# Kernel tuning notes

Hardware: AMD Instinct MI355X
Metric: run time of the kernel (lower is better)

## Reference

```python
import jax, jax.numpy as jnp
import numpy as np

N_NODES = 100000
N_EDGES = 3200000
N_FEAT = 512
NHID = 256
LATENT = 64

def _spmm(edge_index, edge_weight, h, num_nodes):
    # out[dst] = sum_e w_e * h[src_e]  (sparse adj @ h)
    src, dst = edge_index[0], edge_index[1]
    msgs = edge_weight[:, None] * h[src]            # [E, D]
    return jax.ops.segment_sum(msgs, dst, num_segments=num_nodes)

def _gcn_conv(x, edge_index, edge_weight, W, b, num_nodes):
    # GCNConv: adj @ (x @ W) + b
    return _spmm(edge_index, edge_weight, x @ W, num_nodes) + b

def setup_inputs() -> dict:
    key = jax.random.key(0)
    ks = jax.random.split(key, 8)
    x = jax.random.normal(ks[0], (N_NODES, N_FEAT), dtype=jnp.float32)
    edge_index = jax.random.randint(ks[1], (2, N_EDGES), 0, N_NODES, dtype=jnp.int32)
    edge_weight = jax.random.uniform(ks[2], (N_EDGES,), dtype=jnp.float32)
    s1 = 1.0 / np.sqrt(N_FEAT)
    s2 = 1.0 / np.sqrt(NHID)
    W1 = jax.random.normal(ks[3], (N_FEAT, NHID), dtype=jnp.float32) * s1
    b1 = jnp.zeros((NHID,), dtype=jnp.float32)
    W_mu = jax.random.normal(ks[4], (NHID, LATENT), dtype=jnp.float32) * s2
    b_mu = jnp.zeros((LATENT,), dtype=jnp.float32)
    W_logvar = jax.random.normal(ks[5], (NHID, LATENT), dtype=jnp.float32) * s2
    b_logvar = jnp.zeros((LATENT,), dtype=jnp.float32)
    return {"x": x, "edge_index": edge_index, "edge_weight": edge_weight,
            "W1": W1, "b1": b1, "W_mu": W_mu, "b_mu": b_mu,
            "W_logvar": W_logvar, "b_logvar": b_logvar}

def reference(x, edge_index, edge_weight, W1, b1, W_mu, b_mu, W_logvar, b_logvar):
    n = x.shape[0]
    # dropout is identity in eval mode (training=False)
    h = jax.nn.relu(_gcn_conv(x, edge_index, edge_weight, W1, b1, n))  # [N, nhid]
    mu = _gcn_conv(h, edge_index, edge_weight, W_mu, b_mu, n)          # [N, latent]
    logvar = _gcn_conv(h, edge_index, edge_weight, W_logvar, b_logvar, n)
    return (mu, logvar)
```

## Files before the change

### kernel.cpp

```cpp
#include <hip/hip_runtime.h>
#include <hip/hip_bf16.h>

#define NN 100000
#define NE 3200000
#define NF 512
#define NH 256
#define NL 64
#define PAD 40

#define NBKT 256
#define NPB 391
#define CAP 13500
#define NCLS 16
#define DIVC 6250

typedef __bf16 bf16x8 __attribute__((ext_vector_type(8)));
typedef __bf16 bf16x4 __attribute__((ext_vector_type(4)));
typedef __bf16 bf16x2 __attribute__((ext_vector_type(2)));
typedef float  f32x4  __attribute__((ext_vector_type(4)));

__global__ void k_binit2(int* __restrict__ bcur) {
    int t = threadIdx.x;
    bcur[t * 16] = t * CAP;
}

__global__ __launch_bounds__(256) void k_bucket0(const int* __restrict__ src,
                                                 const int* __restrict__ dst,
                                                 const int* __restrict__ wbits,
                                                 int* __restrict__ bcur,
                                                 int2* __restrict__ stage_sw,
                                                 int* __restrict__ stage_d) {
    __shared__ int cnt[NBKT];
    __shared__ int base[NBKT];
    int tid = threadIdx.x;
    cnt[tid] = 0;
    __syncthreads();
    int e0 = blockIdx.x * 1024;
    int ss[4], ww[4], dd[4], lr[4], bb[4];
#pragma unroll
    for (int k = 0; k < 4; k++) {
        int e = e0 + k * 256 + tid;
        int d = dst[e];
        int s = src[e];
        ss[k] = s;
        ww[k] = wbits[e];
        int cls = (int)((unsigned)s / DIVC);
        dd[k] = d | (cls << 20);
        bb[k] = (int)((unsigned)d / NPB);
        lr[k] = atomicAdd(&cnt[bb[k]], 1);
    }
    __syncthreads();
    base[tid] = atomicAdd(&bcur[tid * 16], cnt[tid]);
    __syncthreads();
#pragma unroll
    for (int k = 0; k < 4; k++) {
        int pos = base[bb[k]] + lr[k];
        stage_sw[pos] = make_int2(ss[k], ww[k]);
        stage_d[pos] = dd[k];
    }
}

__global__ void k_bscan(const int* __restrict__ bcur, int* __restrict__ bstart) {
    __shared__ int s[NBKT];
    int t = threadIdx.x;
    int v = bcur[t * 16] - t * CAP;
    s[t] = v;
    __syncthreads();
    for (int off = 1; off < NBKT; off <<= 1) {
        int a = (t >= off) ? s[t - off] : 0;
        __syncthreads();
        s[t] += a;
        __syncthreads();
    }
    bstart[t] = s[t] - v;
    if (t == NBKT - 1) bstart[NBKT] = s[t];
}

__global__ __launch_bounds__(512) void k_build(const int2* __restrict__ stage_sw,
                                               const int* __restrict__ stage_d,
                                               const int* __restrict__ bcur,
                                               const int* __restrict__ bstart,
                                               int* __restrict__ deg,
                                               int* __restrict__ row_ptr,
                                               int2* __restrict__ sedge) {
    __shared__ int hist2[NPB * NCLS];
    __shared__ int sb[2][512];
    int b = blockIdx.x;
    int t = threadIdx.x;
    int n0 = b * NPB;
    int nb = NN - n0; if (nb > NPB) nb = NPB;
    int s0 = b * CAP;
    int fill = bcur[b * 16] - s0;

    for (int i = t; i < nb * NCLS; i += 512) hist2[i] = 0;
    __syncthreads();
    for (int i = t; i < fill; i += 512) {
        int v = stage_d[s0 + i];
        atomicAdd(&hist2[(v & 0xFFFFF) - n0 + ((v >> 20) * 0)], 1);
    }
    __syncthreads();
    for (int i = t; i < nb * NCLS; i += 512) hist2[i] = 0;
    __syncthreads();
    for (int i = t; i < fill; i += 512) {
        int v = stage_d[s0 + i];
        int dn = (v & 0xFFFFF) - n0;
        int c = v >> 20;
        atomicAdd(&hist2[dn * NCLS + c], 1);
    }
    __syncthreads();
    int tot = 0;
    if (t < nb) {
#pragma unroll
        for (int c = 0; c < NCLS; c++) tot += hist2[t * NCLS + c];
    }
    sb[0][t] = (t < nb) ? tot : 0;
    __syncthreads();
    int cur = 0;
    for (int off = 1; off < 512; off <<= 1) {
        int nv = sb[cur][t] + ((t >= off) ? sb[cur][t - off] : 0);
        cur ^= 1;
        sb[cur][t] = nv;
        __syncthreads();
    }
    int base = bstart[b];
    if (t < nb) {
        int acc = base + sb[cur][t] - tot;
        deg[n0 + t] = tot;
        row_ptr[n0 + t] = acc;
#pragma unroll
        for (int c = 0; c < NCLS; c++) {
            int tmp = hist2[t * NCLS + c];
            hist2[t * NCLS + c] = acc;
            acc += tmp;
        }
    }
    __syncthreads();
    for (int i = t; i < fill; i += 512) {
        int v = stage_d[s0 + i];
        int dn = (v & 0xFFFFF) - n0;
        int c = v >> 20;
        int pos = atomicAdd(&hist2[dn * NCLS + c], 1);
        sedge[pos] = stage_sw[s0 + i];
    }
}

__global__ void k_packW1(const float* __restrict__ W, __bf16* __restrict__ P) {
    int i = blockIdx.x * 256 + threadIdx.x;
    int j = i & 7, l = (i >> 3) & 63, kc = (i >> 9) & 15, nt = i >> 13;
    int k = kc * 32 + (l >> 4) * 8 + j;
    int n = nt * 16 + (l & 15);
    P[i] = (__bf16)W[k * NH + n];
}

__global__ void k_packW2(const float* __restrict__ Wmu, const float* __restrict__ Wlv,
                         __bf16* __restrict__ P) {
    int i = blockIdx.x * 256 + threadIdx.x;
    int j = i & 7, l = (i >> 3) & 63, kc = (i >> 9) & 7, nt = i >> 12;
    int k = kc * 32 + (l >> 4) * 8 + j;
    int n = nt * 16 + (l & 15);
    float v = (n < NL) ? Wmu[k * NL + n] : Wlv[k * NL + (n - NL)];
    P[i] = (__bf16)v;
}

__global__ __launch_bounds__(256) void k_gemm1(const float* __restrict__ x,
                                               const __bf16* __restrict__ Wp,
                                               __bf16* __restrict__ T) {
    __shared__ __bf16 As[64 * PAD];
    int tid = threadIdx.x;
    int wv = tid >> 6, lane = tid & 63;
    int quad = lane >> 4, l16 = lane & 15;
    long m0 = (long)blockIdx.x * 64;

    int srow = tid >> 2;
    int scol = (tid & 3) * 8;
    long grow = m0 + srow; if (grow > NN - 1) grow = NN - 1;
    const float* xrow = x + grow * NF;

    f32x4 acc[4][4];
#pragma unroll
    for (int a = 0; a < 4; a++)
#pragma unroll
        for (int b = 0; b < 4; b++) acc[a][b] = (f32x4)0.f;

    float4 p0 = *(const float4*)(xrow + scol);
    float4 p1 = *(const float4*)(xrow + scol + 4);

    for (int kc = 0; kc < 16; kc++) {
        union { bf16x8 v; __bf16 e[8]; } u;
        u.e[0] = (__bf16)p0.x; u.e[1] = (__bf16)p0.y;
        u.e[2] = (__bf16)p0.z; u.e[3] = (__bf16)p0.w;
        u.e[4] = (__bf16)p1.x; u.e[5] = (__bf16)p1.y;
        u.e[6] = (__bf16)p1.z; u.e[7] = (__bf16)p1.w;
        *(bf16x8*)&As[srow * PAD + scol] = u.v;
        __syncthreads();
        if (kc < 15) {
            p0 = *(const float4*)(xrow + (kc + 1) * 32 + scol);
            p1 = *(const float4*)(xrow + (kc + 1) * 32 + scol + 4);
        }
        bf16x8 bfr[4];
#pragma unroll
        for (int nt = 0; nt < 4; nt++)
            bfr[nt] = *(const bf16x8*)(Wp + (((long)(wv * 4 + nt) * 16 + kc) * 64 + lane) * 8);
#pragma unroll
        for (int mt = 0; mt < 4; mt++) {
            bf16x8 af = *(const bf16x8*)&As[(mt * 16 + l16) * PAD + quad * 8];
#pragma unroll
            for (int nt = 0; nt < 4; nt++)
                acc[mt][nt] = __builtin_amdgcn_mfma_f32_16x16x32_bf16(af, bfr[nt], acc[mt][nt], 0, 0, 0);
        }
        __syncthreads();
    }
#pragma unroll
    for (int mt = 0; mt < 4; mt++)
#pragma unroll
        for (int r = 0; r < 4; r++) {
            long gr = m0 + mt * 16 + quad * 4 + r;
            if (gr < NN) {
#pragma unroll
                for (int nt = 0; nt < 4; nt++)
                    T[gr * 256 + wv * 64 + nt * 16 + l16] = (__bf16)acc[mt][nt][r];
            }
        }
}

__global__ __launch_bounds__(256) void k_spmm_h(const __bf16* __restrict__ T,
                                                const int2* __restrict__ sedge,
                                                const int* __restrict__ row_ptr,
                                                const int* __restrict__ deg,
                                                const float* __restrict__ bias,
                                                __bf16* __restrict__ o) {
    int wave = threadIdx.x >> 6, lane = threadIdx.x & 63;
    int n = blockIdx.x * 4 + wave;
    if (n >= NN) return;
    int i = row_ptr[n];
    int end = i + deg[n];
    float a0 = 0.f, a1 = 0.f, a2 = 0.f, a3 = 0.f;
    const bf16x4* base = (const bf16x4*)T;
    for (; i + 8 <= end; i += 8) {
        int2 e0 = sedge[i], e1 = sedge[i+1], e2 = sedge[i+2], e3 = sedge[i+3];
        int2 e4 = sedge[i+4], e5 = sedge[i+5], e6 = sedge[i+6], e7 = sedge[i+7];
        bf16x4 v0 = base[(long)e0.x * 64 + lane];
        bf16x4 v1 = base[(long)e1.x * 64 + lane];
        bf16x4 v2 = base[(long)e2.x * 64 + lane];
        bf16x4 v3 = base[(long)e3.x * 64 + lane];
        bf16x4 v4 = base[(long)e4.x * 64 + lane];
        bf16x4 v5 = base[(long)e5.x * 64 + lane];
        bf16x4 v6 = base[(long)e6.x * 64 + lane];
        bf16x4 v7 = base[(long)e7.x * 64 + lane];
        float w0 = __uint_as_float(e0.y), w1 = __uint_as_float(e1.y);
        float w2 = __uint_as_float(e2.y), w3 = __uint_as_float(e3.y);
        float w4 = __uint_as_float(e4.y), w5 = __uint_as_float(e5.y);
        float w6 = __uint_as_float(e6.y), w7 = __uint_as_float(e7.y);
        a0 += w0*(float)v0[0] + w1*(float)v1[0] + w2*(float)v2[0] + w3*(float)v3[0]
            + w4*(float)v4[0] + w5*(float)v5[0] + w6*(float)v6[0] + w7*(float)v7[0];
        a1 += w0*(float)v0[1] + w1*(float)v1[1] + w2*(float)v2[1] + w3*(float)v3[1]
            + w4*(float)v4[1] + w5*(float)v5[1] + w6*(float)v6[1] + w7*(float)v7[1];
        a2 += w0*(float)v0[2] + w1*(float)v1[2] + w2*(float)v2[2] + w3*(float)v3[2]
            + w4*(float)v4[2] + w5*(float)v5[2] + w6*(float)v6[2] + w7*(float)v7[2];
        a3 += w0*(float)v0[3] + w1*(float)v1[3] + w2*(float)v2[3] + w3*(float)v3[3]
            + w4*(float)v4[3] + w5*(float)v5[3] + w6*(float)v6[3] + w7*(float)v7[3];
    }
    for (; i < end; i++) {
        int2 e = sedge[i];
        float w = __uint_as_float(e.y);
        bf16x4 v = base[(long)e.x * 64 + lane];
        a0 += w*(float)v[0]; a1 += w*(float)v[1];
        a2 += w*(float)v[2]; a3 += w*(float)v[3];
    }
    float4 bv = ((const float4*)bias)[lane];
    bf16x4 ov;
    ov[0] = (__bf16)fmaxf(a0 + bv.x, 0.f);
    ov[1] = (__bf16)fmaxf(a1 + bv.y, 0.f);
    ov[2] = (__bf16)fmaxf(a2 + bv.z, 0.f);
    ov[3] = (__bf16)fmaxf(a3 + bv.w, 0.f);
    ((bf16x4*)o)[(long)n * 64 + lane] = ov;
}

__global__ __launch_bounds__(256) void k_gemm2(const __bf16* __restrict__ h,
                                               const __bf16* __restrict__ Wp,
                                               __bf16* __restrict__ HMb) {
    __shared__ __bf16 As[128 * PAD];
    int tid = threadIdx.x;
    int wv = tid >> 6, lane = tid & 63;
    int quad = lane >> 4, l16 = lane & 15;
    int wr = (wv >> 1) * 64, wc = (wv & 1) * 64;
    long m0 = (long)blockIdx.x * 128;

    int srow = tid >> 1;
    int scol = (tid & 1) * 16;
    long grow = m0 + srow; if (grow > NN - 1) grow = NN - 1;

    f32x4 acc[4][4];
#pragma unroll
    for (int a = 0; a < 4; a++)
#pragma unroll
        for (int b = 0; b < 4; b++) acc[a][b] = (f32x4)0.f;

    const __bf16* rH = h + grow * 256;
    bf16x8 p0 = *(const bf16x8*)(rH + scol);
    bf16x8 p1 = *(const bf16x8*)(rH + scol + 8);

    for (int kc = 0; kc < 8; kc++) {
        *(bf16x8*)&As[srow * PAD + scol] = p0;
        *(bf16x8*)&As[srow * PAD + scol + 8] = p1;
        __syncthreads();
        if (kc < 7) {
            const __bf16* nxt = rH + (kc + 1) * 32;
            p0 = *(const bf16x8*)(nxt + scol);
            p1 = *(const bf16x8*)(nxt + scol + 8);
        }
        bf16x8 bfr[4];
#pragma unroll
        for (int nt = 0; nt < 4; nt++) {
            int ntg = (wc >> 4) + nt;
            bfr[nt] = *(const bf16x8*)(Wp + (((long)ntg * 8 + kc) * 64 + lane) * 8);
        }
#pragma unroll
        for (int mt = 0; mt < 4; mt++) {
            bf16x8 af = *(const bf16x8*)&As[(wr + mt * 16 + l16) * PAD + quad * 8];
#pragma unroll
            for (int nt = 0; nt < 4; nt++)
                acc[mt][nt] = __builtin_amdgcn_mfma_f32_16x16x32_bf16(af, bfr[nt], acc[mt][nt], 0, 0, 0);
        }
        __syncthreads();
    }
#pragma unroll
    for (int mt = 0; mt < 4; mt++)
#pragma unroll
        for (int r = 0; r < 4; r++) {
            long gr = m0 + wr + mt * 16 + quad * 4 + r;
            if (gr < NN) {
#pragma unroll
                for (int nt = 0; nt < 4; nt++)
                    HMb[gr * 128 + wc + nt * 16 + l16] = (__bf16)acc[mt][nt][r];
            }
        }
}

__global__ __launch_bounds__(256) void k_spmm2(const __bf16* __restrict__ HMb,
                                               const int2* __restrict__ sedge,
                                               const int* __restrict__ row_ptr,
                                               const int* __restrict__ deg,
                                               const float* __restrict__ bmu,
                                               const float* __restrict__ blv,
                                               float* __restrict__ out) {
    int wave = threadIdx.x >> 6, lane = threadIdx.x & 63;
    int n = blockIdx.x * 4 + wave;
    if (n >= NN) return;
    int i = row_ptr[n];
    int end = i + deg[n];
    float a0 = 0.f, a1 = 0.f;
    const bf16x2* base = (const bf16x2*)HMb;
    for (; i + 8 <= end; i += 8) {
        int2 e0 = sedge[i], e1 = sedge[i+1], e2 = sedge[i+2], e3 = sedge[i+3];
        int2 e4 = sedge[i+4], e5 = sedge[i+5], e6 = sedge[i+6], e7 = sedge[i+7];
        bf16x2 v0 = base[(long)e0.x * 64 + lane];
        bf16x2 v1 = base[(long)e1.x * 64 + lane];
        bf16x2 v2 = base[(long)e2.x * 64 + lane];
        bf16x2 v3 = base[(long)e3.x * 64 + lane];
        bf16x2 v4 = base[(long)e4.x * 64 + lane];
        bf16x2 v5 = base[(long)e5.x * 64 + lane];
        bf16x2 v6 = base[(long)e6.x * 64 + lane];
        bf16x2 v7 = base[(long)e7.x * 64 + lane];
        a0 += __uint_as_float(e0.y) * (float)v0[0] + __uint_as_float(e1.y) * (float)v1[0]
            + __uint_as_float(e2.y) * (float)v2[0] + __uint_as_float(e3.y) * (float)v3[0]
            + __uint_as_float(e4.y) * (float)v4[0] + __uint_as_float(e5.y) * (float)v5[0]
            + __uint_as_float(e6.y) * (float)v6[0] + __uint_as_float(e7.y) * (float)v7[0];
        a1 += __uint_as_float(e0.y) * (float)v0[1] + __uint_as_float(e1.y) * (float)v1[1]
            + __uint_as_float(e2.y) * (float)v2[1] + __uint_as_float(e3.y) * (float)v3[1]
            + __uint_as_float(e4.y) * (float)v4[1] + __uint_as_float(e5.y) * (float)v5[1]
            + __uint_as_float(e6.y) * (float)v6[1] + __uint_as_float(e7.y) * (float)v7[1];
    }
    for (; i < end; i++) {
        int2 e = sedge[i];
        float w = __uint_as_float(e.y);
        bf16x2 v = base[(long)e.x * 64 + lane];
        a0 += w * (float)v[0]; a1 += w * (float)v[1];
    }
    if (lane < 32) {
        float2 b = ((const float2*)bmu)[lane];
        float2 o = {a0 + b.x, a1 + b.y};
        ((float2*)out)[(long)n * 32 + lane] = o;
    } else {
        float2 b = ((const float2*)blv)[lane - 32];
        float2 o = {a0 + b.x, a1 + b.y};
        ((float2*)(out + (long)NN * NL))[(long)n * 32 + (lane - 32)] = o;
    }
}

extern "C" void kernel_launch(void* const* d_in, const int* in_sizes, int n_in,
                              void* d_out, int out_size, void* d_ws, size_t ws_size,
                              hipStream_t stream) {
    const float* x   = (const float*)d_in[0];
    const int*   ei  = (const int*)d_in[1];
    const float* ew  = (const float*)d_in[2];
    const float* W1  = (const float*)d_in[3];
    const float* b1  = (const float*)d_in[4];
    const float* Wmu = (const float*)d_in[5];
    const float* bmu = (const float*)d_in[6];
    const float* Wlv = (const float*)d_in[7];
    const float* blv = (const float*)d_in[8];
    float* out = (float*)d_out;

    char* ws = (char*)d_ws;
    __bf16* XW     = (__bf16*)(ws);
    __bf16* h      = (__bf16*)(ws + 51200000);
    __bf16* HMb    = (__bf16*)(ws + 102400000);
    int2*  sedge   = (int2*) (ws + 128000000);
    int*   deg     = (int*)  (ws + 153600000);
    int*   row_ptr = (int*)  (ws + 154000000);
    int*   bcur    = (int*)  (ws + 154400000);
    int*   bstart  = (int*)  (ws + 154800000);
    __bf16* Wp1    = (__bf16*)(ws + 154900000);
    __bf16* Wp2    = (__bf16*)(ws + 155200000);

    int2* stage_sw = (int2*)(ws + 51200000);
    int*  stage_d  = (int*) (ws + 51200000 + (long)NBKT * CAP * 8);

    const int* esrc = ei;
    const int* edst = ei + NE;

    k_packW1<<<dim3(512), dim3(256), 0, stream>>>(W1, Wp1);
    k_packW2<<<dim3(128), dim3(256), 0, stream>>>(Wmu, Wlv, Wp2);

    k_binit2<<<dim3(1), dim3(NBKT), 0, stream>>>(bcur);
    k_bucket0<<<dim3(NE / 1024), dim3(256), 0, stream>>>(esrc, edst, (const int*)ew,
                                                         bcur, stage_sw, stage_d);
    k_bscan<<<dim3(1), dim3(NBKT), 0, stream>>>(bcur, bstart);
    k_build<<<dim3(NBKT), dim3(512), 0, stream>>>(stage_sw, stage_d, bcur, bstart,
                                                  deg, row_ptr, sedge);

    k_gemm1<<<dim3((NN + 63) / 64), dim3(256), 0, stream>>>(x, Wp1, XW);
    k_spmm_h<<<dim3((NN + 3) / 4), dim3(256), 0, stream>>>(XW, sedge, row_ptr, deg, b1, h);

    k_gemm2<<<dim3((NN + 127) / 128), dim3(256), 0, stream>>>(h, Wp2, HMb);
    k_spmm2<<<dim3((NN + 3) / 4), dim3(256), 0, stream>>>(HMb, sedge, row_ptr, deg, bmu, blv, out);
}
```

Measured before the change: 842.7 us.

## Process 8-row groups per wave with LDS accumulators, sorting edges by source class

Edges are bucketed into groups of eight destination rows, and within each group sorted by source class, so one wave walks all edges of a group in source-class order. Gathers from the feature tables therefore sweep source nodes more coherently across the group, which should improve cache locality. Per-row partial sums live in LDS and are updated with read-modify-write per edge; the local row index is packed into the high bits of the source field. The cost is an LDS read-modify-write per edge plus serialized dependencies when consecutive edges hit the same row. The bucket count and per-bucket node count change to divide evenly into groups.

Measured after the change: 812.3 us. 1.04x faster.

```diff
diff --git a/kernel.cpp b/kernel.cpp
--- a/kernel.cpp
+++ b/kernel.cpp
@@ -8,20 +8,24 @@
 #define NL 64
 #define PAD 40
 
-#define NBKT 256
-#define NPB 391
-#define CAP 13500
+#define NBKT 250
+#define NPB 400
+#define CAP 13600
 #define NCLS 16
 #define DIVC 6250
+#define RPW 8
+#define SGB 50
+#define NSG 12500
 
 typedef __bf16 bf16x8 __attribute__((ext_vector_type(8)));
 typedef __bf16 bf16x4 __attribute__((ext_vector_type(4)));
 typedef __bf16 bf16x2 __attribute__((ext_vector_type(2)));
 typedef float  f32x4  __attribute__((ext_vector_type(4)));
+typedef float  f32x2  __attribute__((ext_vector_type(2)));
 
 __global__ void k_binit2(int* __restrict__ bcur) {
     int t = threadIdx.x;
-    bcur[t * 16] = t * CAP;
+    if (t < NBKT) bcur[t * 16] = t * CAP;
 }
 
 __global__ __launch_bounds__(256) void k_bucket0(const int* __restrict__ src,
@@ -33,7 +37,7 @@
     __shared__ int cnt[NBKT];
     __shared__ int base[NBKT];
     int tid = threadIdx.x;
-    cnt[tid] = 0;
+    if (tid < NBKT) cnt[tid] = 0;
     __syncthreads();
     int e0 = blockIdx.x * 1024;
     int ss[4], ww[4], dd[4], lr[4], bb[4];
@@ -50,7 +54,7 @@
         lr[k] = atomicAdd(&cnt[bb[k]], 1);
     }
     __syncthreads();
-    base[tid] = atomicAdd(&bcur[tid * 16], cnt[tid]);
+    if (tid < NBKT) base[tid] = atomicAdd(&bcur[tid * 16], cnt[tid]);
     __syncthreads();
 #pragma unroll
     for (int k = 0; k < 4; k++) {
@@ -60,87 +64,75 @@
     }
 }
 
-__global__ void k_bscan(const int* __restrict__ bcur, int* __restrict__ bstart) {
-    __shared__ int s[NBKT];
+__global__ void k_bscan(const int* __restrict__ bcur, int* __restrict__ bstart,
+                        int* __restrict__ run_off) {
+    __shared__ int s[256];
     int t = threadIdx.x;
-    int v = bcur[t * 16] - t * CAP;
+    int v = (t < NBKT) ? (bcur[t * 16] - t * CAP) : 0;
     s[t] = v;
     __syncthreads();
-    for (int off = 1; off < NBKT; off <<= 1) {
+    for (int off = 1; off < 256; off <<= 1) {
         int a = (t >= off) ? s[t - off] : 0;
         __syncthreads();
         s[t] += a;
         __syncthreads();
     }
-    bstart[t] = s[t] - v;
-    if (t == NBKT - 1) bstart[NBKT] = s[t];
+    if (t < NBKT) bstart[t] = s[t] - v;
+    if (t == 0) run_off[NSG * NCLS] = NE;
 }
 
 __global__ __launch_bounds__(512) void k_build(const int2* __restrict__ stage_sw,
                                                const int* __restrict__ stage_d,
                                                const int* __restrict__ bcur,
                                                const int* __restrict__ bstart,
-                                               int* __restrict__ deg,
-                                               int* __restrict__ row_ptr,
+                                               int* __restrict__ run_off,
                                                int2* __restrict__ sedge) {
-    __shared__ int hist2[NPB * NCLS];
-    __shared__ int sb[2][512];
+    __shared__ int hist[SGB * NCLS];
+    __shared__ int sgtot[SGB];
+    __shared__ int sgoff[SGB];
     int b = blockIdx.x;
     int t = threadIdx.x;
     int n0 = b * NPB;
-    int nb = NN - n0; if (nb > NPB) nb = NPB;
     int s0 = b * CAP;
     int fill = bcur[b * 16] - s0;
 
-    for (int i = t; i < nb * NCLS; i += 512) hist2[i] = 0;
+    for (int i = t; i < SGB * NCLS; i += 512) hist[i] = 0;
     __syncthreads();
     for (int i = t; i < fill; i += 512) {
         int v = stage_d[s0 + i];
-        atomicAdd(&hist2[(v & 0xFFFFF) - n0 + ((v >> 20) * 0)], 1);
-    }
-    __syncthreads();
-    for (int i = t; i < nb * NCLS; i += 512) hist2[i] = 0;
+        int d = v & 0xFFFFF, c = v >> 20;
+        atomicAdd(&hist[((d - n0) >> 3) * NCLS + c], 1);
+    }
+    __syncthreads();
+    if (t < SGB) {
+        int sum = 0;
+#pragma unroll
+        for (int c = 0; c < NCLS; c++) sum += hist[t * NCLS + c];
+        sgtot[t] = sum;
+    }
+    __syncthreads();
+    if (t == 0) {
+        int a = 0;
+        for (int sgi = 0; sgi < SGB; sgi++) { sgoff[sgi] = a; a += sgtot[sgi]; }
+    }
+    __syncthreads();
+    if (t < SGB) {
+        int a = bstart[b] + sgoff[t];
+#pragma unroll
+        for (int c = 0; c < NCLS; c++) {
+            int tmp = hist[t * NCLS + c];
+            hist[t * NCLS + c] = a;
+            run_off[(long)(b * SGB + t) * NCLS + c] = a;
+            a += tmp;
+        }
+    }
     __syncthreads();
     for (int i = t; i < fill; i += 512) {
         int v = stage_d[s0 + i];
-        int dn = (v & 0xFFFFF) - n0;
-        int c = v >> 20;
-        atomicAdd(&hist2[dn * NCLS + c], 1);
-    }
-    __syncthreads();
-    int tot = 0;
-    if (t < nb) {
-#pragma unroll
-        for (int c = 0; c < NCLS; c++) tot += hist2[t * NCLS + c];
-    }
-    sb[0][t] = (t < nb) ? tot : 0;
-    __syncthreads();
-    int cur = 0;
-    for (int off = 1; off < 512; off <<= 1) {
-        int nv = sb[cur][t] + ((t >= off) ? sb[cur][t - off] : 0);
-        cur ^= 1;
-        sb[cur][t] = nv;
-        __syncthreads();
-    }
-    int base = bstart[b];
-    if (t < nb) {
-        int acc = base + sb[cur][t] - tot;
-        deg[n0 + t] = tot;
-        row_ptr[n0 + t] = acc;
-#pragma unroll
-        for (int c = 0; c < NCLS; c++) {
-            int tmp = hist2[t * NCLS + c];
-            hist2[t * NCLS + c] = acc;
-            acc += tmp;
-        }
-    }
-    __syncthreads();
-    for (int i = t; i < fill; i += 512) {
-        int v = stage_d[s0 + i];
-        int dn = (v & 0xFFFFF) - n0;
-        int c = v >> 20;
-        int pos = atomicAdd(&hist2[dn * NCLS + c], 1);
-        sedge[pos] = stage_sw[s0 + i];
+        int d = v & 0xFFFFF, c = v >> 20;
+        int pos = atomicAdd(&hist[((d - n0) >> 3) * NCLS + c], 1);
+        int2 sw = stage_sw[s0 + i];
+        sedge[pos] = make_int2(sw.x | ((d & 7) << 20), sw.y);
     }
 }
 
@@ -223,57 +215,66 @@
         }
 }
 
+#define RMW4(EV, VV) { float w = __uint_as_float(EV.y); \
+    f32x4* a = &A[((EV).x >> 20) * 64 + lane]; f32x4 tt = *a; \
+    tt[0] += w * (float)VV[0]; tt[1] += w * (float)VV[1]; \
+    tt[2] += w * (float)VV[2]; tt[3] += w * (float)VV[3]; *a = tt; }
+
 __global__ __launch_bounds__(256) void k_spmm_h(const __bf16* __restrict__ T,
                                                 const int2* __restrict__ sedge,
-                                                const int* __restrict__ row_ptr,
-                                                const int* __restrict__ deg,
+                                                const int* __restrict__ roff,
                                                 const float* __restrict__ bias,
                                                 __bf16* __restrict__ o) {
-    int wave = threadIdx.x >> 6, lane = threadIdx.x & 63;
-    int n = blockIdx.x * 4 + wave;
-    if (n >= NN) return;
-    int i = row_ptr[n];
-    int end = i + deg[n];
-    float a0 = 0.f, a1 = 0.f, a2 = 0.f, a3 = 0.f;
+    __shared__ f32x4 acc[4][RPW][64];
+    int wv = __builtin_amdgcn_readfirstlane(threadIdx.x >> 6);
+    int lane = threadIdx.x & 63;
+    int sg = blockIdx.x * 4 + wv;
+    f32x4* A = &acc[wv][0][0];
+    for (int i = lane; i < RPW * 64; i += 64) A[i] = (f32x4)0.f;
     const bf16x4* base = (const bf16x4*)T;
-    for (; i + 8 <= end; i += 8) {
-        int2 e0 = sedge[i], e1 = sedge[i+1], e2 = sedge[i+2], e3 = sedge[i+3];
-        int2 e4 = sedge[i+4], e5 = sedge[i+5], e6 = sedge[i+6], e7 = sedge[i+7];
-        bf16x4 v0 = base[(long)e0.x * 64 + lane];
-        bf16x4 v1 = base[(long)e1.x * 64 + lane];
-        bf16x4 v2 = base[(long)e2.x * 64 + lane];
-        bf16x4 v3 = base[(long)e3.x * 64 + lane];
-        bf16x4 v4 = base[(long)e4.x * 64 + lane];
-        bf16x4 v5 = base[(long)e5.x * 64 + lane];
-        bf16x4 v6 = base[(long)e6.x * 64 + lane];
-        bf16x4 v7 = base[(long)e7.x * 64 + lane];
-        float w0 = __uint_as_float(e0.y), w1 = __uint_as_float(e1.y);
-        float w2 = __uint_as_float(e2.y), w3 = __uint_as_float(e3.y);
-        float w4 = __uint_as_float(e4.y), w5 = __uint_as_float(e5.y);
-        float w6 = __uint_as_float(e6.y), w7 = __uint_as_float(e7.y);
-        a0 += w0*(float)v0[0] + w1*(float)v1[0] + w2*(float)v2[0] + w3*(float)v3[0]
-            + w4*(float)v4[0] + w5*(float)v5[0] + w6*(float)v6[0] + w7*(float)v7[0];
-        a1 += w0*(float)v0[1] + w1*(float)v1[1] + w2*(float)v2[1] + w3*(float)v3[1]
-            + w4*(float)v4[1] + w5*(float)v5[1] + w6*(float)v6[1] + w7*(float)v7[1];
-        a2 += w0*(float)v0[2] + w1*(float)v1[2] + w2*(float)v2[2] + w3*(float)v3[2]
-            + w4*(float)v4[2] + w5*(float)v5[2] + w6*(float)v6[2] + w7*(float)v7[2];
-        a3 += w0*(float)v0[3] + w1*(float)v1[3] + w2*(float)v2[3] + w3*(float)v3[3]
-            + w4*(float)v4[3] + w5*(float)v5[3] + w6*(float)v6[3] + w7*(float)v7[3];
-    }
-    for (; i < end; i++) {
-        int2 e = sedge[i];
-        float w = __uint_as_float(e.y);
-        bf16x4 v = base[(long)e.x * 64 + lane];
-        a0 += w*(float)v[0]; a1 += w*(float)v[1];
-        a2 += w*(float)v[2]; a3 += w*(float)v[3];
+    for (int c = 0; c < NCLS; c++) {
+        int i = roff[sg * NCLS + c];
+        int e = roff[sg * NCLS + c + 1];
+        for (; i + 8 <= e; i += 8) {
+            int2 e0 = sedge[i], e1 = sedge[i+1], e2 = sedge[i+2], e3 = sedge[i+3];
+            int2 e4 = sedge[i+4], e5 = sedge[i+5], e6 = sedge[i+6], e7 = sedge[i+7];
+            bf16x4 v0 = base[(long)(e0.x & 0xFFFFF) * 64 + lane];
+            bf16x4 v1 = base[(long)(e1.x & 0xFFFFF) * 64 + lane];
+            bf16x4 v2 = base[(long)(e2.x & 0xFFFFF) * 64 + lane];
+            bf16x4 v3 = base[(long)(e3.x & 0xFFFFF) * 64 + lane];
+            bf16x4 v4 = base[(long)(e4.x & 0xFFFFF) * 64 + lane];
+            bf16x4 v5 = base[(long)(e5.x & 0xFFFFF) * 64 + lane];
+            bf16x4 v6 = base[(long)(e6.x & 0xFFFFF) * 64 + lane];
+            bf16x4 v7 = base[(long)(e7.x & 0xFFFFF) * 64 + lane];
+            RMW4(e0, v0) RMW4(e1, v1) RMW4(e2, v2) RMW4(e3, v3)
+            RMW4(e4, v4) RMW4(e5, v5) RMW4(e6, v6) RMW4(e7, v7)
+        }
+        for (; i + 4 <= e; i += 4) {
+            int2 e0 = sedge[i], e1 = sedge[i+1], e2 = sedge[i+2], e3 = sedge[i+3];
+            bf16x4 v0 = base[(long)(e0.x & 0xFFFFF) * 64 + lane];
+            bf16x4 v1 = base[(long)(e1.x & 0xFFFFF) * 64 + lane];
+            bf16x4 v2 = base[(long)(e2.x & 0xFFFFF) * 64 + lane];
+            bf16x4 v3 = base[(long)(e3.x & 0xFFFFF) * 64 + lane];
+            RMW4(e0, v0) RMW4(e1, v1) RMW4(e2, v2) RMW4(e3, v3)
+        }
+        for (; i < e; i++) {
+            int2 e0 = sedge[i];
+            bf16x4 v0 = base[(long)(e0.x & 0xFFFFF) * 64 + lane];
+            RMW4(e0, v0)
+        }
     }
     float4 bv = ((const float4*)bias)[lane];
-    bf16x4 ov;
-    ov[0] = (__bf16)fmaxf(a0 + bv.x, 0.f);
-    ov[1] = (__bf16)fmaxf(a1 + bv.y, 0.f);
-    ov[2] = (__bf16)fmaxf(a2 + bv.z, 0.f);
-    ov[3] = (__bf16)fmaxf(a3 + bv.w, 0.f);
-    ((bf16x4*)o)[(long)n * 64 + lane] = ov;
+    long n0 = (long)sg * RPW;
+#pragma unroll
+    for (int r = 0; r < RPW; r++) {
+        f32x4 t = A[r * 64 + lane];
+        bf16x4 ov;
+        ov[0] = (__bf16)fmaxf(t[0] + bv.x, 0.f);
+        ov[1] = (__bf16)fmaxf(t[1] + bv.y, 0.f);
+        ov[2] = (__bf16)fmaxf(t[2] + bv.z, 0.f);
+        ov[3] = (__bf16)fmaxf(t[3] + bv.w, 0.f);
+        ((bf16x4*)o)[(n0 + r) * 64 + lane] = ov;
+    }
 }
 
 __global__ __launch_bounds__(256) void k_gemm2(const __bf16* __restrict__ h,
@@ -337,54 +338,68 @@
         }
 }
 
+#define RMW2(EV, VV) { float w = __uint_as_float(EV.y); \
+    f32x2* a = &A[((EV).x >> 20) * 64 + lane]; f32x2 tt = *a; \
+    tt[0] += w * (float)VV[0]; tt[1] += w * (float)VV[1]; *a = tt; }
+
 __global__ __launch_bounds__(256) void k_spmm2(const __bf16* __restrict__ HMb,
                                                const int2* __restrict__ sedge,
-                                               const int* __restrict__ row_ptr,
-                                               const int* __restrict__ deg,
+                                               const int* __restrict__ roff,
                                                const float* __restrict__ bmu,
                                                const float* __restrict__ blv,
                                                float* __restrict__ out) {
-    int wave = threadIdx.x >> 6, lane = threadIdx.x & 63;
-    int n = blockIdx.x * 4 + wave;
-    if (n >= NN) return;
-    int i = row_ptr[n];
-    int end = i + deg[n];
-    float a0 = 0.f, a1 = 0.f;
+    __shared__ f32x2 acc[4][RPW][64];
+    int wv = __builtin_amdgcn_readfirstlane(threadIdx.x >> 6);
+    int lane = threadIdx.x & 63;
+    int sg = blockIdx.x * 4 + wv;
+    f32x2* A = &acc[wv][0][0];
+    for (int i = lane; i < RPW * 64; i += 64) A[i] = (f32x2)0.f;
     const bf16x2* base = (const bf16x2*)HMb;
-    for (; i + 8 <= end; i += 8) {
-        int2 e0 = sedge[i], e1 = sedge[i+1], e2 = sedge[i+2], e3 = sedge[i+3];
-        int2 e4 = sedge[i+4], e5 = sedge[i+5], e6 = sedge[i+6], e7 = sedge[i+7];
-        bf16x2 v0 = base[(long)e0.x * 64 + lane];
-        bf16x2 v1 = base[(long)e1.x * 64 + lane];
-        bf16x2 v2 = base[(long)e2.x * 64 + lane];
-        bf16x2 v3 = base[(long)e3.x * 64 + lane];
-        bf16x2 v4 = base[(long)e4.x * 64 + lane];
-        bf16x2 v5 = base[(long)e5.x * 64 + lane];
-        bf16x2 v6 = base[(long)e6.x * 64 + lane];
-        bf16x2 v7 = base[(long)e7.x * 64 + lane];
-        a0 += __uint_as_float(e0.y) * (float)v0[0] + __uint_as_float(e1.y) * (float)v1[0]
-            + __uint_as_float(e2.y) * (float)v2[0] + __uint_as_float(e3.y) * (float)v3[0]
-            + __uint_as_float(e4.y) * (float)v4[0] + __uint_as_float(e5.y) * (float)v5[0]
-            + __uint_as_float(e6.y) * (float)v6[0] + __uint_as_float(e7.y) * (float)v7[0];
-        a1 += __uint_as_float(e0.y) * (float)v0[1] + __uint_as_float(e1.y) * (float)v1[1]
-            + __uint_as_float(e2.y) * (float)v2[1] + __uint_as_float(e3.y) * (float)v3[1]
-            + __uint_as_float(e4.y) * (float)v4[1] + __uint_as_float(e5.y) * (float)v5[1]
-            + __uint_as_float(e6.y) * (float)v6[1] + __uint_as_float(e7.y) * (float)v7[1];
-    }
-    for (; i < end; i++) {
-        int2 e = sedge[i];
-        float w = __uint_as_float(e.y);
-        bf16x2 v = base[(long)e.x * 64 + lane];
-        a0 += w * (float)v[0]; a1 += w * (float)v[1];
-    }
-    if (lane < 32) {
-        float2 b = ((const float2*)bmu)[lane];
-        float2 o = {a0 + b.x, a1 + b.y};
-        ((float2*)out)[(long)n * 32 + lane] = o;
-    } else {
-        float2 b = ((const float2*)blv)[lane - 32];
-        float2 o = {a0 + b.x, a1 + b.y};
-        ((float2*)(out + (long)NN * NL))[(long)n * 32 + (lane - 32)] = o;
+    for (int c = 0; c < NCLS; c++) {
+        int i = roff[sg * NCLS + c];
+        int e = roff[sg * NCLS + c + 1];
+        for (; i + 8 <= e; i += 8) {
+            int2 e0 = sedge[i], e1 = sedge[i+1], e2 = sedge[i+2], e3 = sedge[i+3];
+            int2 e4 = sedge[i+4], e5 = sedge[i+5], e6 = sedge[i+6], e7 = sedge[i+7];
+            bf16x2 v0 = base[(long)(e0.x & 0xFFFFF) * 64 + lane];
+            bf16x2 v1 = base[(long)(e1.x & 0xFFFFF) * 64 + lane];
+            bf16x2 v2 = base[(long)(e2.x & 0xFFFFF) * 64 + lane];
+            bf16x2 v3 = base[(long)(e3.x & 0xFFFFF) * 64 + lane];
+            bf16x2 v4 = base[(long)(e4.x & 0xFFFFF) * 64 + lane];
+            bf16x2 v5 = base[(long)(e5.x & 0xFFFFF) * 64 + lane];
+            bf16x2 v6 = base[(long)(e6.x & 0xFFFFF) * 64 + lane];
+            bf16x2 v7 = base[(long)(e7.x & 0xFFFFF) * 64 + lane];
+            RMW2(e0, v0) RMW2(e1, v1) RMW2(e2, v2) RMW2(e3, v3)
+            RMW2(e4, v4) RMW2(e5, v5) RMW2(e6, v6) RMW2(e7, v7)
+        }
+        for (; i + 4 <= e; i += 4) {
+            int2 e0 = sedge[i], e1 = sedge[i+1], e2 = sedge[i+2], e3 = sedge[i+3];
+            bf16x2 v0 = base[(long)(e0.x & 0xFFFFF) * 64 + lane];
+            bf16x2 v1 = base[(long)(e1.x & 0xFFFFF) * 64 + lane];
+            bf16x2 v2 = base[(long)(e2.x & 0xFFFFF) * 64 + lane];
+            bf16x2 v3 = base[(long)(e3.x & 0xFFFFF) * 64 + lane];
+            RMW2(e0, v0) RMW2(e1, v1) RMW2(e2, v2) RMW2(e3, v3)
+        }
+        for (; i < e; i++) {
+            int2 e0 = sedge[i];
+            bf16x2 v0 = base[(long)(e0.x & 0xFFFFF) * 64 + lane];
+            RMW2(e0, v0)
+        }
+    }
+    long n0 = (long)sg * RPW;
+#pragma unroll
+    for (int r = 0; r < RPW; r++) {
+        f32x2 t = A[r * 64 + lane];
+        float2 o2;
+        if (lane < 32) {
+            float2 b = ((const float2*)bmu)[lane];
+            o2.x = t[0] + b.x; o2.y = t[1] + b.y;
+            ((float2*)out)[(n0 + r) * 32 + lane] = o2;
+        } else {
+            float2 b = ((const float2*)blv)[lane - 32];
+            o2.x = t[0] + b.x; o2.y = t[1] + b.y;
+            ((float2*)(out + (long)NN * NL))[(n0 + r) * 32 + (lane - 32)] = o2;
+        }
     }
 }
 
@@ -407,15 +422,14 @@
     __bf16* h      = (__bf16*)(ws + 51200000);
     __bf16* HMb    = (__bf16*)(ws + 102400000);
     int2*  sedge   = (int2*) (ws + 128000000);
-    int*   deg     = (int*)  (ws + 153600000);
-    int*   row_ptr = (int*)  (ws + 154000000);
-    int*   bcur    = (int*)  (ws + 154400000);
+    int*   run_off = (int*)  (ws + 153600000);
+    int*   bcur    = (int*)  (ws + 154450000);
     int*   bstart  = (int*)  (ws + 154800000);
     __bf16* Wp1    = (__bf16*)(ws + 154900000);
     __bf16* Wp2    = (__bf16*)(ws + 155200000);
 
     int2* stage_sw = (int2*)(ws + 51200000);
-    int*  stage_d  = (int*) (ws + 51200000 + (long)NBKT * CAP * 8);
+    int*  stage_d  = (int*) (ws + 78400000);
 
     const int* esrc = ei;
     const int* edst = ei + NE;
@@ -423,16 +437,16 @@
     k_packW1<<<dim3(512), dim3(256), 0, stream>>>(W1, Wp1);
     k_packW2<<<dim3(128), dim3(256), 0, stream>>>(Wmu, Wlv, Wp2);
 
-    k_binit2<<<dim3(1), dim3(NBKT), 0, stream>>>(bcur);
+    k_binit2<<<dim3(1), dim3(256), 0, stream>>>(bcur);
     k_bucket0<<<dim3(NE / 1024), dim3(256), 0, stream>>>(esrc, edst, (const int*)ew,
                                                          bcur, stage_sw, stage_d);
-    k_bscan<<<dim3(1), dim3(NBKT), 0, stream>>>(bcur, bstart);
+    k_bscan<<<dim3(1), dim3(256), 0, stream>>>(bcur, bstart, run_off);
     k_build<<<dim3(NBKT), dim3(512), 0, stream>>>(stage_sw, stage_d, bcur, bstart,
-                                                  deg, row_ptr, sedge);
+                                                  run_off, sedge);
 
     k_gemm1<<<dim3((NN + 63) / 64), dim3(256), 0, stream>>>(x, Wp1, XW);
-    k_spmm_h<<<dim3((NN + 3) / 4), dim3(256), 0, stream>>>(XW, sedge, row_ptr, deg, b1, h);
+    k_spmm_h<<<dim3(NSG / 4), dim3(256), 0, stream>>>(XW, sedge, run_off, b1, h);
 
     k_gemm2<<<dim3((NN + 127) / 128), dim3(256), 0, stream>>>(h, Wp2, HMb);
-    k_spmm2<<<dim3((NN + 3) / 4), dim3(256), 0, stream>>>(HMb, sedge, row_ptr, deg, bmu, blv, out);
-}
+    k_spmm2<<<dim3(NSG / 4), dim3(256), 0, stream>>>(HMb, sedge, run_off, bmu, blv, out);
+}
```

## Drop source-class sub-sorting in CSR build and restructure SpMM gather unrolling

Applied to the files above, without the earlier changes.

The CSR build no longer sub-sorts each destination row's edges by source class. It also drops the duplicated histogram pass and uses a single per-node histogram with 250 buckets of 400 nodes. Both SpMM kernels switch from 8-way summed-expression unrolling to 16-way array-based gathers with a 4-way tail loop, so more gather loads can be in flight. The trade-off is that losing the source-class ordering may reduce cache locality of the feature gathers, and the larger unroll raises register pressure.

Measured after the change: 821.4 us. 2.5% less time.

```diff
diff --git a/kernel.cpp b/kernel.cpp
--- a/kernel.cpp
+++ b/kernel.cpp
@@ -8,11 +8,9 @@
 #define NL 64
 #define PAD 40
 
-#define NBKT 256
-#define NPB 391
-#define CAP 13500
-#define NCLS 16
-#define DIVC 6250
+#define NBKT 250
+#define NPB 400
+#define CAP 13600
 
 typedef __bf16 bf16x8 __attribute__((ext_vector_type(8)));
 typedef __bf16 bf16x4 __attribute__((ext_vector_type(4)));
@@ -21,7 +19,7 @@
 
 __global__ void k_binit2(int* __restrict__ bcur) {
     int t = threadIdx.x;
-    bcur[t * 16] = t * CAP;
+    if (t < NBKT) bcur[t * 16] = t * CAP;
 }
 
 __global__ __launch_bounds__(256) void k_bucket0(const int* __restrict__ src,
@@ -33,7 +31,7 @@
     __shared__ int cnt[NBKT];
     __shared__ int base[NBKT];
     int tid = threadIdx.x;
-    cnt[tid] = 0;
+    if (tid < NBKT) cnt[tid] = 0;
     __syncthreads();
     int e0 = blockIdx.x * 1024;
     int ss[4], ww[4], dd[4], lr[4], bb[4];
@@ -41,16 +39,14 @@
     for (int k = 0; k < 4; k++) {
         int e = e0 + k * 256 + tid;
         int d = dst[e];
-        int s = src[e];
-        ss[k] = s;
+        ss[k] = src[e];
         ww[k] = wbits[e];
-        int cls = (int)((unsigned)s / DIVC);
-        dd[k] = d | (cls << 20);
+        dd[k] = d;
         bb[k] = (int)((unsigned)d / NPB);
         lr[k] = atomicAdd(&cnt[bb[k]], 1);
     }
     __syncthreads();
-    base[tid] = atomicAdd(&bcur[tid * 16], cnt[tid]);
+    if (tid < NBKT) base[tid] = atomicAdd(&bcur[tid * 16], cnt[tid]);
     __syncthreads();
 #pragma unroll
     for (int k = 0; k < 4; k++) {
@@ -61,19 +57,18 @@
 }
 
 __global__ void k_bscan(const int* __restrict__ bcur, int* __restrict__ bstart) {
-    __shared__ int s[NBKT];
+    __shared__ int s[256];
     int t = threadIdx.x;
-    int v = bcur[t * 16] - t * CAP;
+    int v = (t < NBKT) ? (bcur[t * 16] - t * CAP) : 0;
     s[t] = v;
     __syncthreads();
-    for (int off = 1; off < NBKT; off <<= 1) {
+    for (int off = 1; off < 256; off <<= 1) {
         int a = (t >= off) ? s[t - off] : 0;
         __syncthreads();
         s[t] += a;
         __syncthreads();
     }
-    bstart[t] = s[t] - v;
-    if (t == NBKT - 1) bstart[NBKT] = s[t];
+    if (t < NBKT) bstart[t] = s[t] - v;
 }
 
 __global__ __launch_bounds__(512) void k_build(const int2* __restrict__ stage_sw,
@@ -83,63 +78,40 @@
                                                int* __restrict__ deg,
                                                int* __restrict__ row_ptr,
                                                int2* __restrict__ sedge) {
-    __shared__ int hist2[NPB * NCLS];
+    __shared__ int hist[NPB];
     __shared__ int sb[2][512];
     int b = blockIdx.x;
     int t = threadIdx.x;
     int n0 = b * NPB;
-    int nb = NN - n0; if (nb > NPB) nb = NPB;
     int s0 = b * CAP;
     int fill = bcur[b * 16] - s0;
 
-    for (int i = t; i < nb * NCLS; i += 512) hist2[i] = 0;
+    if (t < NPB) hist[t] = 0;
+    __syncthreads();
+    for (int i = t; i < fill; i += 512)
+        atomicAdd(&hist[stage_d[s0 + i] - n0], 1);
+    __syncthreads();
+    int v = (t < NPB) ? hist[t] : 0;
+    int buf = 0;
+    sb[0][t] = v;
+    __syncthreads();
+    for (int off = 1; off < 512; off <<= 1) {
+        int nv = sb[buf][t] + ((t >= off) ? sb[buf][t - off] : 0);
+        buf ^= 1;
+        sb[buf][t] = nv;
+        __syncthreads();
+    }
+    int base = bstart[b];
+    if (t < NPB) {
+        int abs0 = base + sb[buf][t] - v;
+        deg[n0 + t] = v;
+        row_ptr[n0 + t] = abs0;
+        hist[t] = abs0;
+    }
     __syncthreads();
     for (int i = t; i < fill; i += 512) {
-        int v = stage_d[s0 + i];
-        atomicAdd(&hist2[(v & 0xFFFFF) - n0 + ((v >> 20) * 0)], 1);
-    }
-    __syncthreads();
-    for (int i = t; i < nb * NCLS; i += 512) hist2[i] = 0;
-    __syncthreads();
-    for (int i = t; i < fill; i += 512) {
-        int v = stage_d[s0 + i];
-        int dn = (v & 0xFFFFF) - n0;
-        int c = v >> 20;
-        atomicAdd(&hist2[dn * NCLS + c], 1);
-    }
-    __syncthreads();
-    int tot = 0;
-    if (t < nb) {
-#pragma unroll
-        for (int c = 0; c < NCLS; c++) tot += hist2[t * NCLS + c];
-    }
-    sb[0][t] = (t < nb) ? tot : 0;
-    __syncthreads();
-    int cur = 0;
-    for (int off = 1; off < 512; off <<= 1) {
-        int nv = sb[cur][t] + ((t >= off) ? sb[cur][t - off] : 0);
-        cur ^= 1;
-        sb[cur][t] = nv;
-        __syncthreads();
-    }
-    int base = bstart[b];
-    if (t < nb) {
-        int acc = base + sb[cur][t] - tot;
-        deg[n0 + t] = tot;
-        row_ptr[n0 + t] = acc;
-#pragma unroll
-        for (int c = 0; c < NCLS; c++) {
-            int tmp = hist2[t * NCLS + c];
-            hist2[t * NCLS + c] = acc;
-            acc += tmp;
-        }
-    }
-    __syncthreads();
-    for (int i = t; i < fill; i += 512) {
-        int v = stage_d[s0 + i];
-        int dn = (v & 0xFFFFF) - n0;
-        int c = v >> 20;
-        int pos = atomicAdd(&hist2[dn * NCLS + c], 1);
+        int dl = stage_d[s0 + i] - n0;
+        int pos = atomicAdd(&hist[dl], 1);
         sedge[pos] = stage_sw[s0 + i];
     }
 }
@@ -236,36 +208,44 @@
     int end = i + deg[n];
     float a0 = 0.f, a1 = 0.f, a2 = 0.f, a3 = 0.f;
     const bf16x4* base = (const bf16x4*)T;
-    for (; i + 8 <= end; i += 8) {
-        int2 e0 = sedge[i], e1 = sedge[i+1], e2 = sedge[i+2], e3 = sedge[i+3];
-        int2 e4 = sedge[i+4], e5 = sedge[i+5], e6 = sedge[i+6], e7 = sedge[i+7];
-        bf16x4 v0 = base[(long)e0.x * 64 + lane];
-        bf16x4 v1 = base[(long)e1.x * 64 + lane];
-        bf16x4 v2 = base[(long)e2.x * 64 + lane];
-        bf16x4 v3 = base[(long)e3.x * 64 + lane];
-        bf16x4 v4 = base[(long)e4.x * 64 + lane];
-        bf16x4 v5 = base[(long)e5.x * 64 + lane];
-        bf16x4 v6 = base[(long)e6.x * 64 + lane];
-        bf16x4 v7 = base[(long)e7.x * 64 + lane];
-        float w0 = __uint_as_float(e0.y), w1 = __uint_as_float(e1.y);
-        float w2 = __uint_as_float(e2.y), w3 = __uint_as_float(e3.y);
-        float w4 = __uint_as_float(e4.y), w5 = __uint_as_float(e5.y);
-        float w6 = __uint_as_float(e6.y), w7 = __uint_as_float(e7.y);
-        a0 += w0*(float)v0[0] + w1*(float)v1[0] + w2*(float)v2[0] + w3*(float)v3[0]
-            + w4*(float)v4[0] + w5*(float)v5[0] + w6*(float)v6[0] + w7*(float)v7[0];
-        a1 += w0*(float)v0[1] + w1*(float)v1[1] + w2*(float)v2[1] + w3*(float)v3[1]
-            + w4*(float)v4[1] + w5*(float)v5[1] + w6*(float)v6[1] + w7*(float)v7[1];
-        a2 += w0*(float)v0[2] + w1*(float)v1[2] + w2*(float)v2[2] + w3*(float)v3[2]
-            + w4*(float)v4[2] + w5*(float)v5[2] + w6*(float)v6[2] + w7*(float)v7[2];
-        a3 += w0*(float)v0[3] + w1*(float)v1[3] + w2*(float)v2[3] + w3*(float)v3[3]
-            + w4*(float)v4[3] + w5*(float)v5[3] + w6*(float)v6[3] + w7*(float)v7[3];
+    for (; i + 16 <= end; i += 16) {
+        int2 e[16];
+#pragma unroll
+        for (int k = 0; k < 16; k++) e[k] = sedge[i + k];
+        bf16x4 v[16];
+#pragma unroll
+        for (int k = 0; k < 16; k++) v[k] = base[(long)e[k].x * 64 + lane];
+#pragma unroll
+        for (int k = 0; k < 16; k++) {
+            float w = __uint_as_float(e[k].y);
+            a0 += w * (float)v[k][0];
+            a1 += w * (float)v[k][1];
+            a2 += w * (float)v[k][2];
+            a3 += w * (float)v[k][3];
+        }
+    }
+    for (; i + 4 <= end; i += 4) {
+        int2 e[4];
+#pragma unroll
+        for (int k = 0; k < 4; k++) e[k] = sedge[i + k];
+        bf16x4 v[4];
+#pragma unroll
+        for (int k = 0; k < 4; k++) v[k] = base[(long)e[k].x * 64 + lane];
+#pragma unroll
+        for (int k = 0; k < 4; k++) {
+            float w = __uint_as_float(e[k].y);
+            a0 += w * (float)v[k][0];
+            a1 += w * (float)v[k][1];
+            a2 += w * (float)v[k][2];
+            a3 += w * (float)v[k][3];
+        }
     }
     for (; i < end; i++) {
         int2 e = sedge[i];
         float w = __uint_as_float(e.y);
         bf16x4 v = base[(long)e.x * 64 + lane];
-        a0 += w*(float)v[0]; a1 += w*(float)v[1];
-        a2 += w*(float)v[2]; a3 += w*(float)v[3];
+        a0 += w * (float)v[0]; a1 += w * (float)v[1];
+        a2 += w * (float)v[2]; a3 += w * (float)v[3];
     }
     float4 bv = ((const float4*)bias)[lane];
     bf16x4 ov;
@@ -351,25 +331,33 @@
     int end = i + deg[n];
     float a0 = 0.f, a1 = 0.f;
     const bf16x2* base = (const bf16x2*)HMb;
-    for (; i + 8 <= end; i += 8) {
-        int2 e0 = sedge[i], e1 = sedge[i+1], e2 = sedge[i+2], e3 = sedge[i+3];
-        int2 e4 = sedge[i+4], e5 = sedge[i+5], e6 = sedge[i+6], e7 = sedge[i+7];
-        bf16x2 v0 = base[(long)e0.x * 64 + lane];
-        bf16x2 v1 = base[(long)e1.x * 64 + lane];
-        bf16x2 v2 = base[(long)e2.x * 64 + lane];
-        bf16x2 v3 = base[(long)e3.x * 64 + lane];
-        bf16x2 v4 = base[(long)e4.x * 64 + lane];
-        bf16x2 v5 = base[(long)e5.x * 64 + lane];
-        bf16x2 v6 = base[(long)e6.x * 64 + lane];
-        bf16x2 v7 = base[(long)e7.x * 64 + lane];
-        a0 += __uint_as_float(e0.y) * (float)v0[0] + __uint_as_float(e1.y) * (float)v1[0]
-            + __uint_as_float(e2.y) * (float)v2[0] + __uint_as_float(e3.y) * (float)v3[0]
-            + __uint_as_float(e4.y) * (float)v4[0] + __uint_as_float(e5.y) * (float)v5[0]
-            + __uint_as_float(e6.y) * (float)v6[0] + __uint_as_float(e7.y) * (float)v7[0];
-        a1 += __uint_as_float(e0.y) * (float)v0[1] + __uint_as_float(e1.y) * (float)v1[1]
-            + __uint_as_float(e2.y) * (float)v2[1] + __uint_as_float(e3.y) * (float)v3[1]
-            + __uint_as_float(e4.y) * (float)v4[1] + __uint_as_float(e5.y) * (float)v5[1]
-            + __uint_as_float(e6.y) * (float)v6[1] + __uint_as_float(e7.y) * (float)v7[1];
+    for (; i + 16 <= end; i += 16) {
+        int2 e[16];
+#pragma unroll
+        for (int k = 0; k < 16; k++) e[k] = sedge[i + k];
+        bf16x2 v[16];
+#pragma unroll
+        for (int k = 0; k < 16; k++) v[k] = base[(long)e[k].x * 64 + lane];
+#pragma unroll
+        for (int k = 0; k < 16; k++) {
+            float w = __uint_as_float(e[k].y);
+            a0 += w * (float)v[k][0];
+            a1 += w * (float)v[k][1];
+        }
+    }
+    for (; i + 4 <= end; i += 4) {
+        int2 e[4];
+#pragma unroll
+        for (int k = 0; k < 4; k++) e[k] = sedge[i + k];
+        bf16x2 v[4];
+#pragma unroll
+        for (int k = 0; k < 4; k++) v[k] = base[(long)e[k].x * 64 + lane];
+#pragma unroll
+        for (int k = 0; k < 4; k++) {
+            float w = __uint_as_float(e[k].y);
+            a0 += w * (float)v[k][0];
+            a1 += w * (float)v[k][1];
+        }
     }
     for (; i < end; i++) {
         int2 e = sedge[i];
@@ -415,7 +403,7 @@
     __bf16* Wp2    = (__bf16*)(ws + 155200000);
 
     int2* stage_sw = (int2*)(ws + 51200000);
-    int*  stage_d  = (int*) (ws + 51200000 + (long)NBKT * CAP * 8);
+    int*  stage_d  = (int*) (ws + 78400000);
 
     const int* esrc = ei;
     const int* edst = ei + NE;
@@ -423,10 +411,10 @@
     k_packW1<<<dim3(512), dim3(256), 0, stream>>>(W1, Wp1);
     k_packW2<<<dim3(128), dim3(256), 0, stream>>>(Wmu, Wlv, Wp2);
 
-    k_binit2<<<dim3(1), dim3(NBKT), 0, stream>>>(bcur);
+    k_binit2<<<dim3(1), dim3(256), 0, stream>>>(bcur);
     k_bucket0<<<dim3(NE / 1024), dim3(256), 0, stream>>>(esrc, edst, (const int*)ew,
                                                          bcur, stage_sw, stage_d);
-    k_bscan<<<dim3(1), dim3(NBKT), 0, stream>>>(bcur, bstart);
+    k_bscan<<<dim3(1), dim3(256), 0, stream>>>(bcur, bstart);
     k_build<<<dim3(NBKT), dim3(512), 0, stream>>>(stage_sw, stage_d, bcur, bstart,
                                                   deg, row_ptr, sedge);
 
```
